# Kernel optimization log

Hardware: AMD Instinct MI355X
Metric: run time of the kernel (lower is better)

## Reference

```python
import jax, jax.numpy as jnp
import numpy as np

N_NODES = 8192
N_EDGES = 65536
D_MODEL = 64
D_INNER = 128
D_STATE = 16
DT_RANK = 4
LAYER_NUM = 3
TAU = 0.01


def _unif(key, shape, fan_out):
    stdv = 1.0 / np.sqrt(fan_out)
    return jax.random.uniform(key, shape, jnp.float32, -stdv, stdv)


def setup_inputs() -> dict:
    key = jax.random.key(0)
    ks = jax.random.split(key, 12)
    x = jax.random.normal(ks[0], (N_NODES, D_MODEL), jnp.float32)
    edge_index = jax.random.randint(ks[1], (2, N_EDGES), 0, N_NODES, jnp.int64)
    in_proj_w = _unif(ks[2], (D_MODEL, 2 * D_INNER), 2 * D_INNER)
    x_proj_w = _unif(ks[3], (D_INNER, DT_RANK + 2 * D_STATE), DT_RANK + 2 * D_STATE)
    dt_proj_w = _unif(ks[4], (DT_RANK, D_INNER), D_INNER)
    out_proj_w = _unif(ks[5], (D_INNER, D_MODEL), D_MODEL)
    A_log = jnp.log(jnp.broadcast_to(jnp.arange(1, D_STATE + 1, dtype=jnp.float32)[None, :], (D_INNER, D_STATE)))
    D = jnp.ones((D_INNER,), jnp.float32)
    in_act_w = _unif(ks[6], (D_INNER, 2), 2)
    in_act_b = _unif(ks[7], (2,), 2)
    out_act_w = _unif(ks[8], (D_INNER, 2), 2)
    out_act_b = _unif(ks[9], (2,), 2)
    return {"x": x, "in_proj_w": in_proj_w, "x_proj_w": x_proj_w, "dt_proj_w": dt_proj_w,
            "A_log": A_log, "D": D, "out_proj_w": out_proj_w,
            "in_act_w": in_act_w, "in_act_b": in_act_b, "out_act_w": out_act_w, "out_act_b": out_act_b,
            "edge_index": edge_index, "layer_num": LAYER_NUM}


def _norm_adj(row, col, w, n_nodes):
    # SparseTensor(...).set_diag() adds diag value 1; symmetric deg^-1/2 renorm
    deg = jax.ops.segment_sum(w, row, num_segments=n_nodes) + 1.0
    dinv = jnp.where(deg > 0, deg ** -0.5, 0.0)
    return dinv[row] * w * dinv[col], dinv * dinv  # off-diag edge weights, diag weights


def _spmm(row, col, ew, dw, x, n_nodes):
    # adj @ x with adj = edges(ew) + diag(dw); x: [N, F]
    return jax.ops.segment_sum(ew[:, None] * x[col], row, num_segments=n_nodes) + dw[:, None] * x


def _gumbel_hard(logits, key, tau):
    g = jax.random.gumbel(key, logits.shape, logits.dtype)
    y = jax.nn.softmax((logits + g) / tau, axis=-1)
    hard = jax.nn.one_hot(jnp.argmax(y, axis=-1), logits.shape[-1], dtype=y.dtype)
    return hard + y - jax.lax.stop_gradient(y)


def reference(x, in_proj_w, x_proj_w, dt_proj_w, A_log, D, out_proj_w,
              in_act_w, in_act_b, out_act_w, out_act_b, edge_index, layer_num):
    n_nodes, d_model = x.shape
    d_inner = dt_proj_w.shape[1]
    n = A_log.shape[1]
    dt_rank = dt_proj_w.shape[0]
    row, col = edge_index[0], edge_index[1]

    xl = jnp.broadcast_to(x[:, None, :], (n_nodes, layer_num, d_model))  # [N,L,d_model]
    x_and_res = xl @ in_proj_w                                           # [N,L,2*d_inner]
    xs, res = jnp.split(x_and_res, 2, axis=-1)
    xs = jax.nn.relu(xs)                                                 # u in scan

    A = -jnp.exp(A_log)                                                  # [d_inner, n]
    x_dbl = xs @ x_proj_w                                                # [N,L,dt_rank+2n]
    delta = jax.nn.softplus(x_dbl[..., :dt_rank] @ dt_proj_w)            # [N,L,d_inner]
    B = x_dbl[..., dt_rank:dt_rank + n]                                  # [N,L,n]
    C = x_dbl[..., dt_rank + n:]                                         # [N,L,n]

    deltaA = jnp.exp(jnp.einsum('bld,dn->bldn', delta, A))               # [N,L,d_inner,n]
    deltaB_u = jnp.einsum('bld,bln->bldn', delta * xs, B)                # [N,L,d_inner,n]

    # initial adjacency: unit-weight edges, sym-normalized with self loops
    ew, dw = _norm_adj(row, col, jnp.ones((row.shape[0],), xs.dtype), n_nodes)
    state = jnp.zeros((n_nodes, d_inner, n), xs.dtype)
    gkey = jax.random.key(42)
    ys = []
    for i in range(layer_num):  # small fixed number of GCN/SSM steps
        state = deltaA[:, i] * state + deltaB_u[:, i]
        y = jnp.einsum('bdn,bn->bd', state, C[:, i])                     # [N,d_inner]
        flat = _spmm(row, col, ew, dw, state.reshape(n_nodes, d_inner * n), n_nodes)
        state = flat.reshape(n_nodes, d_inner, n)
        in_p = _gumbel_hard(y @ in_act_w + in_act_b, jax.random.fold_in(gkey, 2 * i), TAU)
        out_p = _gumbel_hard(y @ out_act_w + out_act_b, jax.random.fold_in(gkey, 2 * i + 1), TAU)
        w = in_p[col, 0] * out_p[row, 0]  # keep_in_prob[v] * keep_out_prob[u]
        ew, dw = _norm_adj(row, col, w, n_nodes)
        ys.append(y)

    y = jnp.stack(ys, axis=1) + xs * D                                   # [N,L,d_inner]
    y = y * jax.nn.relu(res)
    out = y @ out_proj_w                                                 # [N,L,d_model]
    return out[:, -1, :]
```

## Files before the change

### kernel.cpp

```cpp
#include <hip/hip_runtime.h>
#include <cstdint>

#define NN 8192
#define NE 65536
#define G 8
#define CAP 64

typedef _Float16 h4 __attribute__((ext_vector_type(4)));

__host__ __device__ inline void tf2x32(uint32_t k0, uint32_t k1,
                                       uint32_t x0, uint32_t x1,
                                       uint32_t& r0, uint32_t& r1) {
  uint32_t ks2 = k0 ^ k1 ^ 0x1BD11BDAu;
  x0 += k0; x1 += k1;
#define TF_ROT(x,d) (((x)<<(d))|((x)>>(32-(d))))
#define TF_R4(ra,rb,rc,rd) \
  x0+=x1; x1=TF_ROT(x1,ra); x1^=x0; \
  x0+=x1; x1=TF_ROT(x1,rb); x1^=x0; \
  x0+=x1; x1=TF_ROT(x1,rc); x1^=x0; \
  x0+=x1; x1=TF_ROT(x1,rd); x1^=x0;
  TF_R4(13,15,26,6)  x0+=k1;  x1+=ks2+1u;
  TF_R4(17,29,16,24) x0+=ks2; x1+=k0+2u;
  TF_R4(13,15,26,6)  x0+=k0;  x1+=k1+3u;
  TF_R4(17,29,16,24) x0+=k1;  x1+=ks2+4u;
  TF_R4(13,15,26,6)  x0+=ks2; x1+=k0+5u;
  r0=x0; r1=x1;
#undef TF_R4
#undef TF_ROT
}

__device__ inline float gumbel32(uint32_t k0, uint32_t k1, uint32_t idx) {
  uint32_t a, b;
  tf2x32(k0, k1, 0u, idx, a, b);
  uint32_t bits = a ^ b;
  float f = __uint_as_float((bits >> 9) | 0x3f800000u) - 1.0f;
  float u = (f > 0.0f) ? f : 1.17549435e-38f;
  return -logf(-logf(u));
}

__global__ void k_zero(int* __restrict__ p, int n) {
  int i = blockIdx.x*blockDim.x + threadIdx.x;
  if (i < n) p[i] = 0;
}

__global__ void k_scatter(const int* __restrict__ ei, int* __restrict__ cnt,
                          int* __restrict__ csr_col) {
  int e = blockIdx.x*blockDim.x + threadIdx.x;
  if (e < NE) {
    int v = ei[e];
    int pos = atomicAdd(&cnt[v], 1);
    if (pos < CAP) csr_col[(v<<6) + pos] = ei[NE + e];
  }
}

__global__ __launch_bounds__(256) void k_nodeprep(
    const float* __restrict__ x, const float* __restrict__ ipw,
    const float* __restrict__ xpw, const float* __restrict__ dtw,
    const float* __restrict__ iaw, const float* __restrict__ iab,
    const float* __restrict__ oaw, const float* __restrict__ oab,
    const int* __restrict__ cnt, const float* __restrict__ alog,
    uint32_t ki0, uint32_t ki1, uint32_t ko0, uint32_t ko1,
    float* __restrict__ xs, float* __restrict__ rres,
    float* __restrict__ delta, float* __restrict__ dxs,
    float* __restrict__ Bm, float* __restrict__ Cm,
    float* __restrict__ inp, float* __restrict__ outp,
    float* __restrict__ dinv0, float* __restrict__ Amat) {
  __shared__ float sx[G][64];
  __shared__ float sxs[G][128];
  __shared__ float sdbl[G][36];
  __shared__ float4 sred4[4];
  int t = threadIdx.x;
  int b0 = blockIdx.x * G;
  if (blockIdx.x == 0) {
    for (int i = t; i < 2048; i += 256) Amat[i] = -expf(alog[i]);
  }
  if (t < G) {
    int v = b0 + t;
    dinv0[v] = 1.0f / sqrtf((float)(min(cnt[v], CAP)) + 1.0f);
  }
  for (int i = t; i < G*64; i += 256) sx[i>>6][i&63] = x[b0*64 + i];
  __syncthreads();
  float acc[G];
#pragma unroll
  for (int g = 0; g < G; g++) acc[g] = 0.f;
  for (int k = 0; k < 64; k++) {
    float w = ipw[k*256 + t];
#pragma unroll
    for (int g = 0; g < G; g++) acc[g] += sx[g][k] * w;
  }
  if (t < 128) {
#pragma unroll
    for (int g = 0; g < G; g++) {
      float v = fmaxf(acc[g], 0.f);
      sxs[g][t] = v;
      xs[(size_t)(b0+g)*128 + t] = v;
    }
  } else {
    int j = t - 128;
#pragma unroll
    for (int g = 0; g < G; g++) rres[(size_t)(b0+g)*128 + j] = fmaxf(acc[g], 0.f);
  }
  __syncthreads();
  for (int idx = t; idx < G*36; idx += 256) {
    int g = idx / 36, c = idx % 36;
    float a = 0.f;
    for (int d = 0; d < 128; d++) a += sxs[g][d] * xpw[d*36 + c];
    sdbl[g][c] = a;
    if (c >= 4 && c < 20)  Bm[(b0+g)*16 + (c-4)]  = a;
    else if (c >= 20)      Cm[(b0+g)*16 + (c-20)] = a;
  }
  __syncthreads();
  int d = t & 127;
  int hi = t >> 7;
  int lane = t & 63, wv = t >> 6;
  for (int gg = 0; gg < 4; gg++) {
    int g = hi*4 + gg;
    int b = b0 + g;
    float dt = sdbl[g][0]*dtw[d]     + sdbl[g][1]*dtw[128+d]
             + sdbl[g][2]*dtw[256+d] + sdbl[g][3]*dtw[384+d];
    float dv = fmaxf(dt, 0.f) + log1pf(expf(-fabsf(dt)));
    delta[(size_t)b*128 + d] = dv;
    float dxv = dv * sxs[g][d];
    dxs[(size_t)b*128 + d] = dxv;
    float4 pr;
    pr.x = dxv * iaw[2*d];   pr.y = dxv * iaw[2*d+1];
    pr.z = dxv * oaw[2*d];   pr.w = dxv * oaw[2*d+1];
    for (int off = 32; off >= 1; off >>= 1) {
      pr.x += __shfl_down(pr.x, off);
      pr.y += __shfl_down(pr.y, off);
      pr.z += __shfl_down(pr.z, off);
      pr.w += __shfl_down(pr.w, off);
    }
    if (lane == 0) sred4[wv] = pr;
    __syncthreads();
    if ((t & 127) == 0) {
      float4 q0 = sred4[hi*2], q1 = sred4[hi*2 + 1];
      float BC = 0.f;
      for (int n = 0; n < 16; n++) BC += sdbl[g][4+n] * sdbl[g][20+n];
      float li0 = BC*(q0.x+q1.x) + iab[0], li1 = BC*(q0.y+q1.y) + iab[1];
      float lo0 = BC*(q0.z+q1.z) + oab[0], lo1 = BC*(q0.w+q1.w) + oab[1];
      uint32_t L0 = 2u*(uint32_t)b, L1 = L0 + 1u;
      inp[b]  = (li0 + gumbel32(ki0, ki1, L0) >= li1 + gumbel32(ki0, ki1, L1)) ? 1.0f : 0.0f;
      outp[b] = (lo0 + gumbel32(ko0, ko1, L0) >= lo1 + gumbel32(ko0, ko1, L1)) ? 1.0f : 0.0f;
    }
    __syncthreads();
  }
}

__global__ __launch_bounds__(256) void k_spmm0f(
    const int* __restrict__ cnt, const int* __restrict__ csr_col,
    const float* __restrict__ dinv,
    const float* __restrict__ inp, const float* __restrict__ outp,
    const float* __restrict__ delta, const float* __restrict__ dxs,
    const float* __restrict__ Bm, const float* __restrict__ Cm,
    const float* __restrict__ Amat,
    _Float16* __restrict__ s_out, float* __restrict__ dinv1,
    float* __restrict__ y2p) {
  __shared__ int   sc[CAP];
  __shared__ float scoef[CAP];
  __shared__ float sgate[CAP];
  __shared__ float sdegs;
  int v = blockIdx.x, t = threadIdx.x;
  int deg = min(cnt[v], CAP);
  if (t < deg) {
    int c = csr_col[(v<<6) + t];
    sc[t] = c; scoef[t] = dinv[c]; sgate[t] = inp[c];
  }
  __syncthreads();
  if (t < 64) {
    float g = (t < deg) ? sgate[t] : 0.f;
    for (int off = 32; off >= 1; off >>= 1) g += __shfl_down(g, off);
    if (t == 0) sdegs = g;
  }
  int d0 = t >> 2, d1 = d0 + 64, nb = t & 3;
  float dv = dinv[v];
  float4 Bv = ((const float4*)(Bm + ((size_t)v << 4)))[nb];
  float dx0 = dxs[v*128 + d0], dx1 = dxs[v*128 + d1];
  float dw = dv * dv;
  float c0 = dw * dx0, c1 = dw * dx1;
  float4 a0 = {c0*Bv.x, c0*Bv.y, c0*Bv.z, c0*Bv.w};
  float4 a1 = {c1*Bv.x, c1*Bv.y, c1*Bv.z, c1*Bv.w};
  for (int j = 0; j < deg; j++) {
    int c = sc[j];
    float coef = dv * scoef[j];
    float4 Bc = ((const float4*)(Bm + ((size_t)c << 4)))[nb];
    float e0 = coef * dxs[c*128 + d0];
    float e1 = coef * dxs[c*128 + d1];
    a0.x += e0*Bc.x; a0.y += e0*Bc.y; a0.z += e0*Bc.z; a0.w += e0*Bc.w;
    a1.x += e1*Bc.x; a1.y += e1*Bc.y; a1.z += e1*Bc.z; a1.w += e1*Bc.w;
  }
  float de0 = delta[v*128 + d0], de1 = delta[v*128 + d1];
  float4 A0 = ((const float4*)(Amat + (d0 << 4)))[nb];
  float4 A1 = ((const float4*)(Amat + (d1 << 4)))[nb];
  float4 E0, E1;
  E0.x = expf(de0*A0.x); E0.y = expf(de0*A0.y); E0.z = expf(de0*A0.z); E0.w = expf(de0*A0.w);
  E1.x = expf(de1*A1.x); E1.y = expf(de1*A1.y); E1.z = expf(de1*A1.z); E1.w = expf(de1*A1.w);
  float4 s0, s1;
  s0.x = E0.x*a0.x + dx0*Bv.x;  s0.y = E0.y*a0.y + dx0*Bv.y;
  s0.z = E0.z*a0.z + dx0*Bv.z;  s0.w = E0.w*a0.w + dx0*Bv.w;
  s1.x = E1.x*a1.x + dx1*Bv.x;  s1.y = E1.y*a1.y + dx1*Bv.y;
  s1.z = E1.z*a1.z + dx1*Bv.z;  s1.w = E1.w*a1.w + dx1*Bv.w;
  if (inp[v] != 0.f) {
    h4* op = (h4*)(s_out + ((size_t)v << 11));
    h4 h0, h1;
    h0.x = (_Float16)s0.x; h0.y = (_Float16)s0.y; h0.z = (_Float16)s0.z; h0.w = (_Float16)s0.w;
    h1.x = (_Float16)s1.x; h1.y = (_Float16)s1.y; h1.z = (_Float16)s1.z; h1.w = (_Float16)s1.w;
    op[t] = h0; op[t + 256] = h1;
  }
  __syncthreads();
  float degs = sdegs;
  float d1v = 1.0f / sqrtf(outp[v]*degs + 1.0f);
  if (t == 0) dinv1[v] = d1v;
  float dw1 = d1v * d1v;
  float4 Cv = ((const float4*)(Cm + ((size_t)v << 4)))[nb];
  float y0p = dw1*(E0.x*s0.x*Cv.x + E0.y*s0.y*Cv.y + E0.z*s0.z*Cv.z + E0.w*s0.w*Cv.w)
            + dx0*(Bv.x*Cv.x + Bv.y*Cv.y + Bv.z*Cv.z + Bv.w*Cv.w);
  float y1p = dw1*(E1.x*s1.x*Cv.x + E1.y*s1.y*Cv.y + E1.z*s1.z*Cv.z + E1.w*s1.w*Cv.w)
            + dx1*(Bv.x*Cv.x + Bv.y*Cv.y + Bv.z*Cv.z + Bv.w*Cv.w);
  y0p += __shfl_xor(y0p, 1); y0p += __shfl_xor(y0p, 2);
  y1p += __shfl_xor(y1p, 1); y1p += __shfl_xor(y1p, 2);
  if (nb == 0) {
    y2p[v*128 + d0] = y0p;
    y2p[v*128 + d1] = y1p;
  }
}

__global__ __launch_bounds__(256) void k_spmm1fo(
    const int* __restrict__ cnt, const int* __restrict__ csr_col,
    const float* __restrict__ dinv1,
    const float* __restrict__ inp, const float* __restrict__ outp,
    const float* __restrict__ delta,
    const float* __restrict__ Cm, const float* __restrict__ Amat,
    const _Float16* __restrict__ s_in, const float* __restrict__ y2p,
    const float* __restrict__ xs, const float* __restrict__ rres,
    const float* __restrict__ Dv, const float* __restrict__ wout,
    float* __restrict__ out) {
  __shared__ int   sc[CAP];
  __shared__ float scoef[CAP];
  __shared__ int   snact;
  __shared__ float ty[128];
  int v = blockIdx.x, t = threadIdx.x;
  if (t == 0) snact = 0;
  __syncthreads();
  int deg = (outp[v] != 0.f) ? min(cnt[v], CAP) : 0;
  if (t < deg) {
    int c = csr_col[(v<<6) + t];
    if (inp[c] != 0.f) {
      int p = atomicAdd(&snact, 1);
      sc[p] = c; scoef[p] = dinv1[c];
    }
  }
  __syncthreads();
  int nact = snact;
  int d0 = t >> 2, d1 = d0 + 64, nb = t & 3;
  float dv = dinv1[v];
  float4 a0 = {0.f,0.f,0.f,0.f}, a1 = {0.f,0.f,0.f,0.f};
  for (int j = 0; j < nact; j++) {
    int c = sc[j];
    float coef = dv * scoef[j];
    const h4* nbp = (const h4*)(s_in + ((size_t)c << 11));
    h4 n0 = nbp[t], n1 = nbp[t + 256];
    a0.x += coef*(float)n0.x; a0.y += coef*(float)n0.y;
    a0.z += coef*(float)n0.z; a0.w += coef*(float)n0.w;
    a1.x += coef*(float)n1.x; a1.y += coef*(float)n1.y;
    a1.z += coef*(float)n1.z; a1.w += coef*(float)n1.w;
  }
  float y0g = 0.f, y1g = 0.f;
  if (nact > 0) {
    float de0 = delta[v*128 + d0], de1 = delta[v*128 + d1];
    float4 A0 = ((const float4*)(Amat + (d0 << 4)))[nb];
    float4 A1 = ((const float4*)(Amat + (d1 << 4)))[nb];
    float4 Cv = ((const float4*)(Cm + ((size_t)v << 4)))[nb];
    y0g = expf(de0*A0.x)*a0.x*Cv.x + expf(de0*A0.y)*a0.y*Cv.y +
          expf(de0*A0.z)*a0.z*Cv.z + expf(de0*A0.w)*a0.w*Cv.w;
    y1g = expf(de1*A1.x)*a1.x*Cv.x + expf(de1*A1.y)*a1.y*Cv.y +
          expf(de1*A1.z)*a1.z*Cv.z + expf(de1*A1.w)*a1.w*Cv.w;
  }
  y0g += __shfl_xor(y0g, 1); y0g += __shfl_xor(y0g, 2);
  y1g += __shfl_xor(y1g, 1); y1g += __shfl_xor(y1g, 2);
  if (nb == 0) {
    float yA = y0g + y2p[v*128 + d0];
    float yB = y1g + y2p[v*128 + d1];
    ty[d0] = (yA + xs[v*128 + d0]*Dv[d0]) * rres[v*128 + d0];
    ty[d1] = (yB + xs[v*128 + d1]*Dv[d1]) * rres[v*128 + d1];
  }
  __syncthreads();
  if (t < 64) {
    float acc = 0.f;
    for (int d = 0; d < 128; d++) acc += ty[d] * wout[d*64 + t];
    out[v*64 + t] = acc;
  }
}

extern "C" void kernel_launch(void* const* d_in, const int* in_sizes, int n_in,
                              void* d_out, int out_size, void* d_ws, size_t ws_size,
                              hipStream_t stream) {
  const float* x    = (const float*)d_in[0];
  const float* ipw  = (const float*)d_in[1];
  const float* xpw  = (const float*)d_in[2];
  const float* dtw  = (const float*)d_in[3];
  const float* alog = (const float*)d_in[4];
  const float* Dv   = (const float*)d_in[5];
  const float* wout = (const float*)d_in[6];
  const float* iaw  = (const float*)d_in[7];
  const float* iab  = (const float*)d_in[8];
  const float* oaw  = (const float*)d_in[9];
  const float* oab  = (const float*)d_in[10];
  const int*   ei   = (const int*)d_in[11];
  (void)in_sizes; (void)n_in; (void)out_size; (void)ws_size;

  float* W = (float*)d_ws;
  size_t o = 0;
  float* xs    = W + o; o += (size_t)NN*128;
  float* rres  = W + o; o += (size_t)NN*128;
  float* delta = W + o; o += (size_t)NN*128;
  float* dxs   = W + o; o += (size_t)NN*128;
  float* y2p   = W + o; o += (size_t)NN*128;
  float* Bm    = W + o; o += (size_t)NN*16;
  float* Cm    = W + o; o += (size_t)NN*16;
  float* Amat  = W + o; o += 2048;
  float* dinv0 = W + o; o += NN;
  float* dinv1 = W + o; o += NN;
  float* inp   = W + o; o += NN;
  float* outp  = W + o; o += NN;
  _Float16* stA = (_Float16*)(W + o); o += (size_t)NN*1024;
  int* cnt     = (int*)(W + o);
  int* csr_col = cnt + NN;

  uint32_t ki0, ki1, ko0, ko1;
  tf2x32(0u, 42u, 0u, 0u, ki0, ki1);
  tf2x32(0u, 42u, 0u, 1u, ko0, ko1);

  k_zero<<<NN/256, 256, 0, stream>>>(cnt, NN);
  k_scatter<<<NE/256, 256, 0, stream>>>(ei, cnt, csr_col);

  k_nodeprep<<<NN/G, 256, 0, stream>>>(x, ipw, xpw, dtw, iaw, iab, oaw, oab,
                                       cnt, alog, ki0, ki1, ko0, ko1,
                                       xs, rres, delta, dxs, Bm, Cm, inp, outp,
                                       dinv0, Amat);

  k_spmm0f<<<NN, 256, 0, stream>>>(cnt, csr_col, dinv0, inp, outp,
                                   delta, dxs, Bm, Cm, Amat, stA, dinv1, y2p);

  k_spmm1fo<<<NN, 256, 0, stream>>>(cnt, csr_col, dinv1, inp, outp,
                                    delta, Cm, Amat, stA, y2p,
                                    xs, rres, Dv, wout, (float*)d_out);
}
```

Before: 174.3 us.

## Store dxs and B in fp16 for spmm gather, inline dinv0, double nodeprep group

```diff
diff --git a/kernel.cpp b/kernel.cpp
--- a/kernel.cpp
+++ b/kernel.cpp
@@ -3,10 +3,11 @@
 
 #define NN 8192
 #define NE 65536
-#define G 8
+#define G 16
 #define CAP 64
 
 typedef _Float16 h4 __attribute__((ext_vector_type(4)));
+typedef _Float16 h2 __attribute__((ext_vector_type(2)));
 
 __host__ __device__ inline void tf2x32(uint32_t k0, uint32_t k1,
                                        uint32_t x0, uint32_t x1,
@@ -58,25 +59,23 @@
     const float* __restrict__ xpw, const float* __restrict__ dtw,
     const float* __restrict__ iaw, const float* __restrict__ iab,
     const float* __restrict__ oaw, const float* __restrict__ oab,
-    const int* __restrict__ cnt, const float* __restrict__ alog,
+    const float* __restrict__ alog,
     uint32_t ki0, uint32_t ki1, uint32_t ko0, uint32_t ko1,
     float* __restrict__ xs, float* __restrict__ rres,
-    float* __restrict__ delta, float* __restrict__ dxs,
-    float* __restrict__ Bm, float* __restrict__ Cm,
+    float* __restrict__ delta, _Float16* __restrict__ dxh2,
+    float* __restrict__ Bm, _Float16* __restrict__ Bh,
+    float* __restrict__ Cm,
     float* __restrict__ inp, float* __restrict__ outp,
-    float* __restrict__ dinv0, float* __restrict__ Amat) {
+    float* __restrict__ Amat) {
   __shared__ float sx[G][64];
   __shared__ float sxs[G][128];
   __shared__ float sdbl[G][36];
+  __shared__ float sdx[2][128];
   __shared__ float4 sred4[4];
   int t = threadIdx.x;
   int b0 = blockIdx.x * G;
   if (blockIdx.x == 0) {
     for (int i = t; i < 2048; i += 256) Amat[i] = -expf(alog[i]);
-  }
-  if (t < G) {
-    int v = b0 + t;
-    dinv0[v] = 1.0f / sqrtf((float)(min(cnt[v], CAP)) + 1.0f);
   }
   for (int i = t; i < G*64; i += 256) sx[i>>6][i&63] = x[b0*64 + i];
   __syncthreads();
@@ -106,22 +105,24 @@
     float a = 0.f;
     for (int d = 0; d < 128; d++) a += sxs[g][d] * xpw[d*36 + c];
     sdbl[g][c] = a;
-    if (c >= 4 && c < 20)  Bm[(b0+g)*16 + (c-4)]  = a;
-    else if (c >= 20)      Cm[(b0+g)*16 + (c-20)] = a;
+    if (c >= 4 && c < 20) {
+      Bm[(b0+g)*16 + (c-4)] = a;
+      Bh[(b0+g)*16 + (c-4)] = (_Float16)a;
+    } else if (c >= 20)    Cm[(b0+g)*16 + (c-20)] = a;
   }
   __syncthreads();
   int d = t & 127;
   int hi = t >> 7;
   int lane = t & 63, wv = t >> 6;
-  for (int gg = 0; gg < 4; gg++) {
-    int g = hi*4 + gg;
+  for (int gg = 0; gg < G/2; gg++) {
+    int g = hi*(G/2) + gg;
     int b = b0 + g;
     float dt = sdbl[g][0]*dtw[d]     + sdbl[g][1]*dtw[128+d]
              + sdbl[g][2]*dtw[256+d] + sdbl[g][3]*dtw[384+d];
     float dv = fmaxf(dt, 0.f) + log1pf(expf(-fabsf(dt)));
     delta[(size_t)b*128 + d] = dv;
     float dxv = dv * sxs[g][d];
-    dxs[(size_t)b*128 + d] = dxv;
+    sdx[hi][d] = dxv;
     float4 pr;
     pr.x = dxv * iaw[2*d];   pr.y = dxv * iaw[2*d+1];
     pr.z = dxv * oaw[2*d];   pr.w = dxv * oaw[2*d+1];
@@ -133,7 +134,13 @@
     }
     if (lane == 0) sred4[wv] = pr;
     __syncthreads();
-    if ((t & 127) == 0) {
+    if (d < 64) {
+      h2 pk;
+      pk.x = (_Float16)sdx[hi][d];
+      pk.y = (_Float16)sdx[hi][d + 64];
+      ((h2*)(dxh2 + ((size_t)b << 7)))[d] = pk;
+    }
+    if (d == 0) {
       float4 q0 = sred4[hi*2], q1 = sred4[hi*2 + 1];
       float BC = 0.f;
       for (int n = 0; n < 16; n++) BC += sdbl[g][4+n] * sdbl[g][20+n];
@@ -149,11 +156,10 @@
 
 __global__ __launch_bounds__(256) void k_spmm0f(
     const int* __restrict__ cnt, const int* __restrict__ csr_col,
-    const float* __restrict__ dinv,
     const float* __restrict__ inp, const float* __restrict__ outp,
-    const float* __restrict__ delta, const float* __restrict__ dxs,
-    const float* __restrict__ Bm, const float* __restrict__ Cm,
-    const float* __restrict__ Amat,
+    const float* __restrict__ delta, const _Float16* __restrict__ dxh2,
+    const float* __restrict__ Bm, const _Float16* __restrict__ Bh,
+    const float* __restrict__ Cm, const float* __restrict__ Amat,
     _Float16* __restrict__ s_out, float* __restrict__ dinv1,
     float* __restrict__ y2p) {
   __shared__ int   sc[CAP];
@@ -164,7 +170,9 @@
   int deg = min(cnt[v], CAP);
   if (t < deg) {
     int c = csr_col[(v<<6) + t];
-    sc[t] = c; scoef[t] = dinv[c]; sgate[t] = inp[c];
+    sc[t] = c;
+    scoef[t] = 1.0f / sqrtf((float)min(cnt[c], CAP) + 1.0f);
+    sgate[t] = inp[c];
   }
   __syncthreads();
   if (t < 64) {
@@ -173,9 +181,10 @@
     if (t == 0) sdegs = g;
   }
   int d0 = t >> 2, d1 = d0 + 64, nb = t & 3;
-  float dv = dinv[v];
+  float dv = 1.0f / sqrtf((float)deg + 1.0f);
   float4 Bv = ((const float4*)(Bm + ((size_t)v << 4)))[nb];
-  float dx0 = dxs[v*128 + d0], dx1 = dxs[v*128 + d1];
+  h2 pkv = ((const h2*)(dxh2 + ((size_t)v << 7)))[d0];
+  float dx0 = (float)pkv.x, dx1 = (float)pkv.y;
   float dw = dv * dv;
   float c0 = dw * dx0, c1 = dw * dx1;
   float4 a0 = {c0*Bv.x, c0*Bv.y, c0*Bv.z, c0*Bv.w};
@@ -183,11 +192,13 @@
   for (int j = 0; j < deg; j++) {
     int c = sc[j];
     float coef = dv * scoef[j];
-    float4 Bc = ((const float4*)(Bm + ((size_t)c << 4)))[nb];
-    float e0 = coef * dxs[c*128 + d0];
-    float e1 = coef * dxs[c*128 + d1];
-    a0.x += e0*Bc.x; a0.y += e0*Bc.y; a0.z += e0*Bc.z; a0.w += e0*Bc.w;
-    a1.x += e1*Bc.x; a1.y += e1*Bc.y; a1.z += e1*Bc.z; a1.w += e1*Bc.w;
+    h2 pk = ((const h2*)(dxh2 + ((size_t)c << 7)))[d0];
+    h4 Bp = ((const h4*)(Bh + ((size_t)c << 4)))[nb];
+    float e0 = coef * (float)pk.x;
+    float e1 = coef * (float)pk.y;
+    float bx = (float)Bp.x, by = (float)Bp.y, bz = (float)Bp.z, bw = (float)Bp.w;
+    a0.x += e0*bx; a0.y += e0*by; a0.z += e0*bz; a0.w += e0*bw;
+    a1.x += e1*bx; a1.y += e1*by; a1.z += e1*bz; a1.w += e1*bw;
   }
   float de0 = delta[v*128 + d0], de1 = delta[v*128 + d1];
   float4 A0 = ((const float4*)(Amat + (d0 << 4)))[nb];
@@ -314,16 +325,16 @@
   float* xs    = W + o; o += (size_t)NN*128;
   float* rres  = W + o; o += (size_t)NN*128;
   float* delta = W + o; o += (size_t)NN*128;
-  float* dxs   = W + o; o += (size_t)NN*128;
   float* y2p   = W + o; o += (size_t)NN*128;
   float* Bm    = W + o; o += (size_t)NN*16;
   float* Cm    = W + o; o += (size_t)NN*16;
   float* Amat  = W + o; o += 2048;
-  float* dinv0 = W + o; o += NN;
   float* dinv1 = W + o; o += NN;
   float* inp   = W + o; o += NN;
   float* outp  = W + o; o += NN;
-  _Float16* stA = (_Float16*)(W + o); o += (size_t)NN*1024;
+  _Float16* dxh2 = (_Float16*)(W + o); o += (size_t)NN*64;
+  _Float16* Bh   = (_Float16*)(W + o); o += (size_t)NN*8;
+  _Float16* stA  = (_Float16*)(W + o); o += (size_t)NN*1024;
   int* cnt     = (int*)(W + o);
   int* csr_col = cnt + NN;
 
@@ -335,12 +346,13 @@
   k_scatter<<<NE/256, 256, 0, stream>>>(ei, cnt, csr_col);
 
   k_nodeprep<<<NN/G, 256, 0, stream>>>(x, ipw, xpw, dtw, iaw, iab, oaw, oab,
-                                       cnt, alog, ki0, ki1, ko0, ko1,
-                                       xs, rres, delta, dxs, Bm, Cm, inp, outp,
-                                       dinv0, Amat);
-
-  k_spmm0f<<<NN, 256, 0, stream>>>(cnt, csr_col, dinv0, inp, outp,
-                                   delta, dxs, Bm, Cm, Amat, stA, dinv1, y2p);
+                                       alog, ki0, ki1, ko0, ko1,
+                                       xs, rres, delta, dxh2, Bm, Bh, Cm,
+                                       inp, outp, Amat);
+
+  k_spmm0f<<<NN, 256, 0, stream>>>(cnt, csr_col, inp, outp,
+                                   delta, dxh2, Bm, Bh, Cm, Amat,
+                                   stA, dinv1, y2p);
 
   k_spmm1fo<<<NN, 256, 0, stream>>>(cnt, csr_col, dinv1, inp, outp,
                                     delta, Cm, Amat, stA, y2p,
```

Result: slower. 181.3 us (+4.0%).
